# Performance work log

Hardware: AMD Instinct MI355X
Metric: run time of the kernel (lower is better)

Reference implementation:

```python
import jax, jax.numpy as jnp
import numpy as np

T = 2048          # num tokens (prefill)
H = 4096          # hidden_size
NH = 32           # num query heads
NKV = 8           # num kv heads (GQA)
HD = H // NH      # head_dim = 128
BASE = 1000000.0  # rope_theta
NEG = -1e30


def _rope(x, positions):
    # NeoX-style rotary embedding (vLLM default). x: [T, nh, HD]
    half = HD // 2
    inv_freq = 1.0 / (BASE ** (jnp.arange(half, dtype=jnp.float32) / half))
    freqs = positions.astype(jnp.float32)[:, None] * inv_freq  # [T, half]
    cos = jnp.concatenate([jnp.cos(freqs), jnp.cos(freqs)], -1)[:, None, :]
    sin = jnp.concatenate([jnp.sin(freqs), jnp.sin(freqs)], -1)[:, None, :]
    rot = jnp.concatenate([-x[..., half:], x[..., :half]], -1)
    return x * cos + rot * sin


def setup_inputs() -> dict:
    key = jax.random.key(0)
    k1, k2, k3 = jax.random.split(key, 3)
    hidden_states = jax.random.normal(k1, (T, H), jnp.float32)
    wqkv = jax.random.normal(k2, (H, (NH + 2 * NKV) * HD), jnp.float32) * 0.02
    wo = jax.random.normal(k3, (NH * HD, H), jnp.float32) * 0.02
    positions = jnp.arange(T, dtype=jnp.int32)
    return {"positions": positions, "hidden_states": hidden_states,
            "wqkv": wqkv, "wo": wo}


def reference(positions, hidden_states, wqkv, wo):
    # fused QKV projection
    qkv = hidden_states @ wqkv                      # [T, (NH+2*NKV)*HD]
    q, k, v = jnp.split(qkv, [NH * HD, NH * HD + NKV * HD], axis=-1)
    q = q.reshape(T, NH, HD)
    k = k.reshape(T, NKV, HD)
    v = v.reshape(T, NKV, HD)
    # inline RoPE on q, k
    q = _rope(q, positions)
    k = _rope(k, positions)
    # GQA: expand kv heads to query heads
    rep = NH // NKV
    k = jnp.repeat(k, rep, axis=1)                  # [T, NH, HD]
    v = jnp.repeat(v, rep, axis=1)
    # causal scaled dot-product attention (prefill path of PagedAttention)
    scores = jnp.einsum('qhd,khd->hqk', q, k) * (HD ** -0.5)  # [NH, T, T]
    causal = positions[:, None] >= positions[None, :]          # [T, T]
    scores = jnp.where(causal[None, :, :], scores, NEG)
    probs = jax.nn.softmax(scores, axis=-1)
    attn = jnp.einsum('hqk,khd->qhd', probs, v).reshape(T, NH * HD)
    return attn @ wo
```

## Files before the change

kernel.cpp:

```cpp
#include <hip/hip_runtime.h>
#include <hip/hip_bf16.h>

typedef __attribute__((ext_vector_type(8))) short bf16x8;
typedef __attribute__((ext_vector_type(4))) float f32x4;
typedef unsigned short u16;

#define T_TOK 2048
#define HID 4096
#define NH 32
#define NKV 8
#define HD 128
#define QKVN 6144
#define KOFF 4096
#define VOFF 5120
#define QSCALE (0.08838834764831845f * 1.4426950408889634f)
#define THR_LOG2 11.0f

static __device__ __forceinline__ float bf2f(u16 x) {
    union { float f; unsigned u; } v; v.u = ((unsigned)x) << 16; return v.f;
}
static __device__ __forceinline__ u16 f2bf(float f) {
    union { float f; unsigned u; } v; v.f = f;
    unsigned u = v.u;
    unsigned r = (u + 0x7fff + ((u >> 16) & 1)) >> 16;
    return (u16)r;
}

static __device__ __forceinline__ void gload16(const u16* g, u16* l) {
    __builtin_amdgcn_global_load_lds((const __attribute__((address_space(1))) void*)g,
                                     (__attribute__((address_space(3))) void*)l, 16, 0, 0);
}

#define VMC(n) asm volatile("s_waitcnt vmcnt(%0)" :: "i"(n) : "memory")
#define LGKM0() asm volatile("s_waitcnt lgkmcnt(0)" ::: "memory")
#define BAR() __builtin_amdgcn_s_barrier()
#define SCHB() __builtin_amdgcn_sched_barrier(0)

__global__ __launch_bounds__(256) void prepk(const float* __restrict__ hs, u16* __restrict__ hsb,
                                             const float* __restrict__ wqkv, u16* __restrict__ wqkvT,
                                             const float* __restrict__ wo, u16* __restrict__ woT) {
    __shared__ float tile[64][65];
    int by = blockIdx.y;
    int tid = threadIdx.x;
    if (by >= 64) {
        int b = blockIdx.x + 160 * (by - 64);
        for (int i = b * 256 + tid; i < (T_TOK * HID / 4); i += 1280 * 256) {
            float4 v = ((const float4*)hs)[i];
            ushort4 o;
            o.x = f2bf(v.x); o.y = f2bf(v.y); o.z = f2bf(v.z); o.w = f2bf(v.w);
            ((ushort4*)hsb)[i] = o;
        }
        return;
    }
    int bx = blockIdx.x;
    const float* in; u16* out; int C, c0;
    if (bx < 96) { in = wqkv; out = wqkvT; C = QKVN; c0 = bx * 64; }
    else         { in = wo;   out = woT;   C = HID;  c0 = (bx - 96) * 64; }
    int R = HID;
    int r0 = by * 64;
#pragma unroll
    for (int it = 0; it < 4; ++it) {
        int ci = it * 256 + tid;
        int r = ci >> 4, c4 = (ci & 15) * 4;
        float4 v = *(const float4*)&in[(size_t)(r0 + r) * C + c0 + c4];
        tile[r][c4 + 0] = v.x; tile[r][c4 + 1] = v.y; tile[r][c4 + 2] = v.z; tile[r][c4 + 3] = v.w;
    }
    __syncthreads();
#pragma unroll
    for (int it = 0; it < 4; ++it) {
        int ci = it * 256 + tid;
        int c = ci >> 4, rq = (ci & 15) * 4;
        ushort4 o;
        o.x = f2bf(tile[rq + 0][c]); o.y = f2bf(tile[rq + 1][c]);
        o.z = f2bf(tile[rq + 2][c]); o.w = f2bf(tile[rq + 3][c]);
        *(ushort4*)&out[(size_t)(c0 + c) * R + r0 + rq] = o;
    }
}

template <int BN, int OUTF32>
__global__ __launch_bounds__(512) void gemm8p(const u16* __restrict__ A, const u16* __restrict__ Bt,
                                              void* __restrict__ Cout, int M, int N, int K) {
    constexpr int BM = 256, BK = 32;
    constexpr int WN = BN / 2;
    constexpr int NF = WN / 16;
    constexpr int BCH = BN / 16;
    constexpr int CA = 2 + (BCH + 7) / 8;
    constexpr int CB = 2 + BCH / 8;
    constexpr int ABUF = BM * BK;
    constexpr int BBUF = BN * BK;
    constexpr int BUFSZ = ABUF + BBUF;

    __shared__ __attribute__((aligned(16))) u16 lds[4 * BUFSZ];

    int bid = blockIdx.x;
    int m0 = ((bid >> 3) & 7) * BM;
    int n0 = ((bid & 7) * 4 + (bid >> 6)) * BN;
    int tid = threadIdx.x, lane = tid & 63, wid = tid >> 6;
    int wm = wid >> 1, wn = wid & 1;
    int l15 = lane & 15, g4 = lane >> 4;
    int srow = lane >> 2;
    int sslot = (lane & 3) ^ ((lane >> 3) & 3);
    int swz = (g4 ^ ((l15 >> 1) & 3)) * 8;
    int NK = K / BK;
    bool shortw = (CA != CB) && (wid >= 4);

    auto STAGE = [&](int kt, int c) {
        u16* base = &lds[(kt & 3) * BUFSZ];
        size_t kcol = (size_t)kt * BK + sslot * 8;
        if (c < 2) {
            int ch = wid * 2 + c;
            gload16(&A[(size_t)(m0 + ch * 16 + srow) * K + kcol], base + ch * 512);
        } else {
            int ch = (c - 2) * 8 + wid;
            if (ch < BCH)
                gload16(&Bt[(size_t)(n0 + ch * 16 + srow) * K + kcol], base + ABUF + ch * 512);
        }
    };

    f32x4 acc[4][NF];
#pragma unroll
    for (int i = 0; i < 4; ++i)
#pragma unroll
        for (int j = 0; j < NF; ++j) acc[i][j] = (f32x4){0.f, 0.f, 0.f, 0.f};

    for (int t = 0; t < 3; ++t)
        for (int c = 0; c < CA; ++c) STAGE(t, c);
    if (shortw) VMC(2 * CB); else VMC(2 * CA);
    BAR(); SCHB();

    for (int g = 0; g < NK; ++g) {
        const u16* ab = &lds[(g & 3) * BUFSZ];
        const u16* bb = ab + ABUF;

        bf16x8 bfr[NF], af0, af1;
#pragma unroll
        for (int j = 0; j < NF; ++j)
            bfr[j] = *(const bf16x8*)&bb[(wn * WN + j * 16 + l15) * BK + swz];
        af0 = *(const bf16x8*)&ab[(wm * 64 + 0 * 16 + l15) * BK + swz];
        af1 = *(const bf16x8*)&ab[(wm * 64 + 1 * 16 + l15) * BK + swz];
        if (g + 3 < NK) {
            STAGE(g + 3, 0); STAGE(g + 3, 1);
        }
        __builtin_amdgcn_s_setprio(1);
#pragma unroll
        for (int j = 0; j < NF; ++j) {
            acc[0][j] = __builtin_amdgcn_mfma_f32_16x16x32_bf16(af0, bfr[j], acc[0][j], 0, 0, 0);
            acc[1][j] = __builtin_amdgcn_mfma_f32_16x16x32_bf16(af1, bfr[j], acc[1][j], 0, 0, 0);
        }
        __builtin_amdgcn_s_setprio(0);

        bf16x8 af2, af3;
        af2 = *(const bf16x8*)&ab[(wm * 64 + 2 * 16 + l15) * BK + swz];
        af3 = *(const bf16x8*)&ab[(wm * 64 + 3 * 16 + l15) * BK + swz];
        if (g + 3 < NK) {
#pragma unroll
            for (int c = 2; c < CA; ++c) STAGE(g + 3, c);
        }
        __builtin_amdgcn_s_setprio(1);
#pragma unroll
        for (int j = 0; j < NF; ++j) {
            acc[2][j] = __builtin_amdgcn_mfma_f32_16x16x32_bf16(af2, bfr[j], acc[2][j], 0, 0, 0);
            acc[3][j] = __builtin_amdgcn_mfma_f32_16x16x32_bf16(af3, bfr[j], acc[3][j], 0, 0, 0);
        }
        __builtin_amdgcn_s_setprio(0);

        if (g < NK - 3)       { if (shortw) VMC(2 * CB); else VMC(2 * CA); }
        else if (g == NK - 3) { if (shortw) VMC(CB);     else VMC(CA); }
        else if (g == NK - 2) VMC(0);
        BAR(); SCHB();
    }

#pragma unroll
    for (int mi = 0; mi < 4; ++mi)
#pragma unroll
        for (int j = 0; j < NF; ++j)
#pragma unroll
            for (int i = 0; i < 4; ++i) {
                int row = m0 + wm * 64 + mi * 16 + g4 * 4 + i;
                int col = n0 + wn * WN + j * 16 + l15;
                float v = acc[mi][j][i];
                if (OUTF32) ((float*)Cout)[(size_t)row * N + col] = v;
                else        ((u16*)Cout)[(size_t)row * N + col] = f2bf(v);
            }
}

template <int BN, int OUTF32>
__global__ __launch_bounds__(512) void gemm4p(const u16* __restrict__ A, const u16* __restrict__ Bt,
                                              void* __restrict__ Cout, int M, int N, int K) {
    constexpr int NF = BN / 64;
    constexpr int LB = BN / 128;
    constexpr int DBUF = (128 + BN) * 64;
    constexpr int BHALF = (BN / 2) * 64;
    __shared__ __attribute__((aligned(16))) u16 lds[2 * DBUF];

    int bid = blockIdx.x;
    int m0 = ((bid >> 3) & 15) * 128;
    int n0 = ((bid & 7) * 2 + (bid >> 7)) * BN;
    int tid = threadIdx.x, lane = tid & 63, wid = tid >> 6;
    int wm = wid >> 2, wn = wid & 3;
    int l15 = lane & 15, g4 = lane >> 4;
    int sw = l15 & 7;
    int srow = tid >> 3;
    int sslot8 = (((tid & 7) ^ ((tid >> 3) & 7))) * 8;
    int brow0 = (wn & 1) * (BN / 4);
    int NK = K / 64;

    auto STAGE_A = [&](int kt, int h) {
        gload16(&A[(size_t)(m0 + h * 64 + srow) * K + kt * 64 + sslot8],
                &lds[(kt & 1) * DBUF + h * 4096 + wid * 512]);
    };
    auto STAGE_B = [&](int kt, int bh) {
#pragma unroll
        for (int it = 0; it < LB; ++it)
            gload16(&Bt[(size_t)(n0 + bh * (BN / 2) + it * 64 + srow) * K + kt * 64 + sslot8],
                    &lds[(kt & 1) * DBUF + 8192 + bh * BHALF + it * 4096 + wid * 512]);
    };

    f32x4 acc[4][NF];
#pragma unroll
    for (int i = 0; i < 4; ++i)
#pragma unroll
        for (int j = 0; j < NF; ++j) acc[i][j] = (f32x4){0.f, 0.f, 0.f, 0.f};

    STAGE_A(0, 0); STAGE_A(0, 1); STAGE_B(0, 0); STAGE_B(0, 1);
    STAGE_A(1, 0); STAGE_A(1, 1); STAGE_B(1, 0); STAGE_B(1, 1);
    VMC(2 + 2 * LB);
    BAR(); SCHB();

    for (int g = 0; g < NK; ++g) {
        const u16* dd = &lds[(g & 1) * DBUF];
        const u16* aw = dd + wm * 4096;
        const u16* bw = dd + 8192 + (wn >> 1) * BHALF;
        bool mid = (g > 0) && (g + 1 < NK);
        bf16x8 bfr[NF], af0, af1;

#pragma unroll
        for (int nf = 0; nf < NF; ++nf)
            bfr[nf] = *(const bf16x8*)&bw[(brow0 + nf * 16 + l15) * 64 + ((g4 ^ sw) * 8)];
        af0 = *(const bf16x8*)&aw[(0 * 16 + l15) * 64 + ((g4 ^ sw) * 8)];
        af1 = *(const bf16x8*)&aw[(1 * 16 + l15) * 64 + ((g4 ^ sw) * 8)];
        if (mid) STAGE_A(g + 1, 0);
        BAR(); LGKM0();
        __builtin_amdgcn_s_setprio(1);
#pragma unroll
        for (int nf = 0; nf < NF; ++nf) {
            acc[0][nf] = __builtin_amdgcn_mfma_f32_16x16x32_bf16(af0, bfr[nf], acc[0][nf], 0, 0, 0);
            acc[1][nf] = __builtin_amdgcn_mfma_f32_16x16x32_bf16(af1, bfr[nf], acc[1][nf], 0, 0, 0);
        }
        __builtin_amdgcn_s_setprio(0);
        BAR();

        af0 = *(const bf16x8*)&aw[(2 * 16 + l15) * 64 + ((g4 ^ sw) * 8)];
        af1 = *(const bf16x8*)&aw[(3 * 16 + l15) * 64 + ((g4 ^ sw) * 8)];
        if (mid) STAGE_B(g + 1, 1);
        BAR(); LGKM0();
        __builtin_amdgcn_s_setprio(1);
#pragma unroll
        for (int nf = 0; nf < NF; ++nf) {
            acc[2][nf] = __builtin_amdgcn_mfma_f32_16x16x32_bf16(af0, bfr[nf], acc[2][nf], 0, 0, 0);
            acc[3][nf] = __builtin_amdgcn_mfma_f32_16x16x32_bf16(af1, bfr[nf], acc[3][nf], 0, 0, 0);
        }
        __builtin_amdgcn_s_setprio(0);
        BAR();

#pragma unroll
        for (int nf = 0; nf < NF; ++nf)
            bfr[nf] = *(const bf16x8*)&bw[(brow0 + nf * 16 + l15) * 64 + (((4 + g4) ^ sw) * 8)];
        af0 = *(const bf16x8*)&aw[(0 * 16 + l15) * 64 + (((4 + g4) ^ sw) * 8)];
        af1 = *(const bf16x8*)&aw[(1 * 16 + l15) * 64 + (((4 + g4) ^ sw) * 8)];
        if (mid) STAGE_A(g + 1, 1);
        BAR(); LGKM0();
        __builtin_amdgcn_s_setprio(1);
#pragma unroll
        for (int nf = 0; nf < NF; ++nf) {
            acc[0][nf] = __builtin_amdgcn_mfma_f32_16x16x32_bf16(af0, bfr[nf], acc[0][nf], 0, 0, 0);
            acc[1][nf] = __builtin_amdgcn_mfma_f32_16x16x32_bf16(af1, bfr[nf], acc[1][nf], 0, 0, 0);
        }
        __builtin_amdgcn_s_setprio(0);
        BAR();

        af0 = *(const bf16x8*)&aw[(2 * 16 + l15) * 64 + (((4 + g4) ^ sw) * 8)];
        af1 = *(const bf16x8*)&aw[(3 * 16 + l15) * 64 + (((4 + g4) ^ sw) * 8)];
        if (g + 2 < NK) STAGE_B(g + 2, 0);
        BAR(); LGKM0();
        __builtin_amdgcn_s_setprio(1);
#pragma unroll
        for (int nf = 0; nf < NF; ++nf) {
            acc[2][nf] = __builtin_amdgcn_mfma_f32_16x16x32_bf16(af0, bfr[nf], acc[2][nf], 0, 0, 0);
            acc[3][nf] = __builtin_amdgcn_mfma_f32_16x16x32_bf16(af1, bfr[nf], acc[3][nf], 0, 0, 0);
        }
        __builtin_amdgcn_s_setprio(0);
        if (g <= NK - 3)      VMC(LB);
        else if (g == NK - 2) VMC(0);
        BAR(); SCHB();
    }

#pragma unroll
    for (int mf = 0; mf < 4; ++mf)
#pragma unroll
        for (int nf = 0; nf < NF; ++nf)
#pragma unroll
            for (int i = 0; i < 4; ++i) {
                int row = m0 + wm * 64 + mf * 16 + g4 * 4 + i;
                int col = n0 + wn * (BN / 4) + nf * 16 + l15;
                float v = acc[mf][nf][i];
                if (OUTF32) ((float*)Cout)[(size_t)row * N + col] = v;
                else        ((u16*)Cout)[(size_t)row * N + col] = f2bf(v);
            }
}

__global__ __launch_bounds__(256) void ropevtk(u16* __restrict__ qkvb, const int* __restrict__ positions,
                                               u16* __restrict__ vT) {
    __shared__ __attribute__((aligned(16))) u16 tile[64][136];
    int bx = blockIdx.x;
    int tid = threadIdx.x;
    if (bx < 2048) {
        __shared__ float cs_[64], sn_[64];
        int t = bx;
        float pos = (float)positions[t];
        if (tid < 64) {
            int d = tid;
            float inv = exp2f(-(float)d * (19.931568569324174f / 64.0f));
            float fr = pos * inv;
            cs_[d] = cosf(fr);
            sn_[d] = sinf(fr);
        }
        __syncthreads();
#pragma unroll
        for (int it = 0; it < 10; ++it) {
            int ci = it * 256 + tid;
            int hh = ci >> 6, d = ci & 63;
            int base = (hh < NH) ? hh * HD : KOFF + (hh - NH) * HD;
            size_t off = (size_t)t * QKVN + base + d;
            float x1 = bf2f(qkvb[off]);
            float x2 = bf2f(qkvb[off + 64]);
            float s = sn_[d], c = cs_[d];
            float y1 = x1 * c - x2 * s;
            float y2 = x2 * c + x1 * s;
            if (hh < NH) { y1 *= QSCALE; y2 *= QSCALE; }
            qkvb[off]      = f2bf(y1);
            qkvb[off + 64] = f2bf(y2);
        }
        return;
    }
    int idx = bx - 2048;
    int kvh = idx >> 5, t0 = (idx & 31) * 64;
#pragma unroll
    for (int it = 0; it < 4; ++it) {
        int ci = it * 256 + tid;
        int r = ci >> 4, c8 = (ci & 15) * 8;
        *(bf16x8*)&tile[r][c8] = *(const bf16x8*)&qkvb[(size_t)(t0 + r) * QKVN + VOFF + kvh * HD + c8];
    }
    __syncthreads();
#pragma unroll
    for (int it = 0; it < 4; ++it) {
        int ci = it * 256 + tid;
        int d = ci >> 3, tc = (ci & 7) * 8;
        union { bf16x8 v; u16 u[8]; } o;
#pragma unroll
        for (int e = 0; e < 8; ++e) o.u[e] = tile[tc + e][d];
        *(bf16x8*)&vT[((size_t)kvh * HD + d) * T_TOK + t0 + tc] = o.v;
    }
}

__global__ __launch_bounds__(512) void attnk(const u16* __restrict__ qkvb, const u16* __restrict__ vT,
                                             u16* __restrict__ attnb) {
    __shared__ __attribute__((aligned(16))) u16 kt_[64 * 132];
    __shared__ __attribute__((aligned(16))) u16 vt_[128 * 68];
    __shared__ __attribute__((aligned(16))) u16 pl_[8 * 16 * 68];
    int h = blockIdx.x, qt = 15 - blockIdx.y;
    int kvh = h >> 2;
    int q0 = qt * 128;
    int tid = threadIdx.x, lane = tid & 63, wid = tid >> 6;
    int l15 = lane & 15, g = lane >> 4;

    const u16* kbase = qkvb + KOFF + (size_t)kvh * HD;
    const u16* vbase = vT + (size_t)kvh * HD * T_TOK;

    bf16x8 qf[4];
    int qrow = q0 + wid * 16 + l15;
#pragma unroll
    for (int ks = 0; ks < 4; ++ks)
        qf[ks] = *(const bf16x8*)&qkvb[(size_t)qrow * QKVN + h * HD + ks * 32 + g * 8];

    f32x4 o[8];
#pragma unroll
    for (int df = 0; df < 8; ++df) o[df] = (f32x4){0.f, 0.f, 0.f, 0.f};
    float m_run[4], l_run[4];
#pragma unroll
    for (int i = 0; i < 4; ++i) { m_run[i] = -3.0e38f; l_run[i] = 0.f; }

    int NT = 2 * qt + 2;

    bf16x8 kreg[2], vreg[2];
#pragma unroll
    for (int it = 0; it < 2; ++it) {
        int gi = it * 512 + tid;
        kreg[it] = *(const bf16x8*)&kbase[(size_t)(gi >> 4) * QKVN + (gi & 15) * 8];
        vreg[it] = *(const bf16x8*)&vbase[(size_t)(gi >> 3) * T_TOK + (gi & 7) * 8];
    }
#pragma unroll
    for (int it = 0; it < 2; ++it) {
        int gi = it * 512 + tid;
        *(bf16x8*)&kt_[(gi >> 4) * 132 + (gi & 15) * 8] = kreg[it];
        *(bf16x8*)&vt_[(gi >> 3) * 68 + (gi & 7) * 8] = vreg[it];
    }
#pragma unroll
    for (int it = 0; it < 2; ++it) {
        int gi = it * 512 + tid;
        kreg[it] = *(const bf16x8*)&kbase[(size_t)(64 + (gi >> 4)) * QKVN + (gi & 15) * 8];
        vreg[it] = *(const bf16x8*)&vbase[(size_t)(gi >> 3) * T_TOK + 64 + (gi & 7) * 8];
    }
    __syncthreads();

    for (int kt2 = 0; kt2 < NT; ++kt2) {
        int kvb = kt2 * 64;
        bool active = (kvb <= q0 + wid * 16 + 15);
        bool diag   = (kvb + 63 > q0 + wid * 16);

        if (active) {
            f32x4 s[4];
#pragma unroll
            for (int nf = 0; nf < 4; ++nf) s[nf] = (f32x4){0.f, 0.f, 0.f, 0.f};
            __builtin_amdgcn_s_setprio(1);
#pragma unroll
            for (int ks = 0; ks < 4; ++ks) {
#pragma unroll
                for (int nf = 0; nf < 4; ++nf) {
                    bf16x8 bfr = *(const bf16x8*)&kt_[(nf * 16 + l15) * 132 + ks * 32 + g * 8];
                    s[nf] = __builtin_amdgcn_mfma_f32_16x16x32_bf16(qf[ks], bfr, s[nf], 0, 0, 0);
                }
            }
            __builtin_amdgcn_s_setprio(0);

            float mloc[4];
#pragma unroll
            for (int i = 0; i < 4; ++i) {
                int qr = q0 + wid * 16 + g * 4 + i;
                float mx = -3.0e38f;
#pragma unroll
                for (int nf = 0; nf < 4; ++nf) {
                    float v = s[nf][i];
                    if (diag) {
                        int kvc = kvb + nf * 16 + l15;
                        v = (kvc <= qr) ? v : -1.0e30f;
                        s[nf][i] = v;
                    }
                    mx = fmaxf(mx, v);
                }
                mloc[i] = mx;
            }

            int ok = 1;
#pragma unroll
            for (int i = 0; i < 4; ++i) ok &= (mloc[i] <= m_run[i] + THR_LOG2) ? 1 : 0;
            if (!__all(ok)) {
                float mrow[4];
#pragma unroll
                for (int i = 0; i < 4; ++i) mrow[i] = mloc[i];
#pragma unroll
                for (int dd = 1; dd < 16; dd <<= 1)
#pragma unroll
                    for (int i = 0; i < 4; ++i) mrow[i] = fmaxf(mrow[i], __shfl_xor(mrow[i], dd));
                float alpha[4];
#pragma unroll
                for (int i = 0; i < 4; ++i) {
                    float mnew = fmaxf(m_run[i], mrow[i]);
                    alpha[i] = exp2f(m_run[i] - mnew);
                    m_run[i] = mnew;
                    l_run[i] *= alpha[i];
                }
#pragma unroll
                for (int df = 0; df < 8; ++df)
#pragma unroll
                    for (int i = 0; i < 4; ++i) o[df][i] *= alpha[i];
            }

#pragma unroll
            for (int nf = 0; nf < 4; ++nf)
#pragma unroll
                for (int i = 0; i < 4; ++i) {
                    float p = exp2f(s[nf][i] - m_run[i]);
                    l_run[i] += p;
                    pl_[wid * 1088 + (g * 4 + i) * 68 + nf * 16 + l15] = f2bf(p);
                }

            __builtin_amdgcn_s_setprio(1);
#pragma unroll
            for (int ks2 = 0; ks2 < 2; ++ks2) {
                bf16x8 af = *(const bf16x8*)&pl_[wid * 1088 + l15 * 68 + ks2 * 32 + g * 8];
#pragma unroll
                for (int df = 0; df < 8; ++df) {
                    bf16x8 bfr = *(const bf16x8*)&vt_[(df * 16 + l15) * 68 + ks2 * 32 + g * 8];
                    o[df] = __builtin_amdgcn_mfma_f32_16x16x32_bf16(af, bfr, o[df], 0, 0, 0);
                }
            }
            __builtin_amdgcn_s_setprio(0);
        }

        if (kt2 < NT - 1) {
            __syncthreads();
#pragma unroll
            for (int it = 0; it < 2; ++it) {
                int gi = it * 512 + tid;
                *(bf16x8*)&kt_[(gi >> 4) * 132 + (gi & 15) * 8] = kreg[it];
                *(bf16x8*)&vt_[(gi >> 3) * 68 + (gi & 7) * 8] = vreg[it];
            }
            int ktl = (kt2 + 2 < NT) ? kt2 + 2 : NT - 1;
#pragma unroll
            for (int it = 0; it < 2; ++it) {
                int gi = it * 512 + tid;
                kreg[it] = *(const bf16x8*)&kbase[(size_t)(ktl * 64 + (gi >> 4)) * QKVN + (gi & 15) * 8];
                vreg[it] = *(const bf16x8*)&vbase[(size_t)(gi >> 3) * T_TOK + ktl * 64 + (gi & 7) * 8];
            }
            __syncthreads();
        }
    }

#pragma unroll
    for (int dd = 1; dd < 16; dd <<= 1)
#pragma unroll
        for (int i = 0; i < 4; ++i) l_run[i] += __shfl_xor(l_run[i], dd);

#pragma unroll
    for (int df = 0; df < 8; ++df)
#pragma unroll
        for (int i = 0; i < 4; ++i) {
            int qr = q0 + wid * 16 + g * 4 + i;
            int col = h * HD + df * 16 + l15;
            attnb[(size_t)qr * (NH * HD) + col] = f2bf(o[df][i] / l_run[i]);
        }
}

extern "C" void kernel_launch(void* const* d_in, const int* in_sizes, int n_in,
                              void* d_out, int out_size, void* d_ws, size_t ws_size,
                              hipStream_t stream) {
    const int*   positions = (const int*)d_in[0];
    const float* hs        = (const float*)d_in[1];
    const float* wqkv      = (const float*)d_in[2];
    const float* wo        = (const float*)d_in[3];
    float* out = (float*)d_out;

    char* ws = (char*)d_ws;
    u16* hsb   = (u16*)(ws);
    u16* wqkvT = (u16*)(ws + 16777216);
    u16* woT   = (u16*)(ws + 16777216 + 50331648);
    u16* qkvb  = (u16*)(ws + 16777216 + 50331648 + 33554432);
    u16* vT    = (u16*)(ws + 16777216 + 50331648 + 33554432 + 25165824);
    u16* attnb = hsb;

    prepk<<<dim3(160, 72), 256, 0, stream>>>(hs, hsb, wqkv, wqkvT, wo, woT);

    gemm8p<192, 0><<<dim3(256), 512, 0, stream>>>(hsb, wqkvT, qkvb, T_TOK, QKVN, HID);

    ropevtk<<<dim3(2048 + 256), 256, 0, stream>>>(qkvb, positions, vT);

    attnk<<<dim3(NH, 16), 512, 0, stream>>>(qkvb, vT, attnb);

    gemm4p<256, 1><<<dim3(256), 512, 0, stream>>>(attnb, woT, out, T_TOK, HID, HID);
}
```

Before: 313.0 us.

## Split attention KV range across two blocks and merge with a combine kernel

The causal attention kernel now splits each query tile's key range into two halves handled by separate blocks (grid z=2). Each block writes a partial normalized output plus its running max and sum, and a new combine kernel merges the halves with log-sum-exp weights. This doubles the block count and shortens the longest per-block loop, which improves load balance and occupancy across CUs. The cost is an extra launch and an extra round trip of partial outputs through memory, and the partials are stored in bf16 before combining.

```diff
diff --git a/kernel.cpp b/kernel.cpp
--- a/kernel.cpp
+++ b/kernel.cpp
@@ -364,16 +364,20 @@
 }
 
 __global__ __launch_bounds__(512) void attnk(const u16* __restrict__ qkvb, const u16* __restrict__ vT,
-                                             u16* __restrict__ attnb) {
+                                             u16* __restrict__ Opart, float* __restrict__ mlp) {
     __shared__ __attribute__((aligned(16))) u16 kt_[64 * 132];
     __shared__ __attribute__((aligned(16))) u16 vt_[128 * 68];
     __shared__ __attribute__((aligned(16))) u16 pl_[8 * 16 * 68];
     int h = blockIdx.x, qt = 15 - blockIdx.y;
+    int z = blockIdx.z;
     int kvh = h >> 2;
     int q0 = qt * 128;
     int tid = threadIdx.x, lane = tid & 63, wid = tid >> 6;
     int l15 = lane & 15, g = lane >> 4;
 
+    int tb = z * (qt + 1);
+    int te = tb + qt + 1;
+
     const u16* kbase = qkvb + KOFF + (size_t)kvh * HD;
     const u16* vbase = vT + (size_t)kvh * HD * T_TOK;
 
@@ -390,14 +394,12 @@
 #pragma unroll
     for (int i = 0; i < 4; ++i) { m_run[i] = -3.0e38f; l_run[i] = 0.f; }
 
-    int NT = 2 * qt + 2;
-
     bf16x8 kreg[2], vreg[2];
 #pragma unroll
     for (int it = 0; it < 2; ++it) {
         int gi = it * 512 + tid;
-        kreg[it] = *(const bf16x8*)&kbase[(size_t)(gi >> 4) * QKVN + (gi & 15) * 8];
-        vreg[it] = *(const bf16x8*)&vbase[(size_t)(gi >> 3) * T_TOK + (gi & 7) * 8];
+        kreg[it] = *(const bf16x8*)&kbase[(size_t)(tb * 64 + (gi >> 4)) * QKVN + (gi & 15) * 8];
+        vreg[it] = *(const bf16x8*)&vbase[(size_t)(gi >> 3) * T_TOK + tb * 64 + (gi & 7) * 8];
     }
 #pragma unroll
     for (int it = 0; it < 2; ++it) {
@@ -405,15 +407,18 @@
         *(bf16x8*)&kt_[(gi >> 4) * 132 + (gi & 15) * 8] = kreg[it];
         *(bf16x8*)&vt_[(gi >> 3) * 68 + (gi & 7) * 8] = vreg[it];
     }
-#pragma unroll
-    for (int it = 0; it < 2; ++it) {
-        int gi = it * 512 + tid;
-        kreg[it] = *(const bf16x8*)&kbase[(size_t)(64 + (gi >> 4)) * QKVN + (gi & 15) * 8];
-        vreg[it] = *(const bf16x8*)&vbase[(size_t)(gi >> 3) * T_TOK + 64 + (gi & 7) * 8];
+    {
+        int ktl = (tb + 1 < te) ? tb + 1 : te - 1;
+#pragma unroll
+        for (int it = 0; it < 2; ++it) {
+            int gi = it * 512 + tid;
+            kreg[it] = *(const bf16x8*)&kbase[(size_t)(ktl * 64 + (gi >> 4)) * QKVN + (gi & 15) * 8];
+            vreg[it] = *(const bf16x8*)&vbase[(size_t)(gi >> 3) * T_TOK + ktl * 64 + (gi & 7) * 8];
+        }
     }
     __syncthreads();
 
-    for (int kt2 = 0; kt2 < NT; ++kt2) {
+    for (int kt2 = tb; kt2 < te; ++kt2) {
         int kvb = kt2 * 64;
         bool active = (kvb <= q0 + wid * 16 + 15);
         bool diag   = (kvb + 63 > q0 + wid * 16);
@@ -498,7 +503,7 @@
             __builtin_amdgcn_s_setprio(0);
         }
 
-        if (kt2 < NT - 1) {
+        if (kt2 < te - 1) {
             __syncthreads();
 #pragma unroll
             for (int it = 0; it < 2; ++it) {
@@ -506,7 +511,7 @@
                 *(bf16x8*)&kt_[(gi >> 4) * 132 + (gi & 15) * 8] = kreg[it];
                 *(bf16x8*)&vt_[(gi >> 3) * 68 + (gi & 7) * 8] = vreg[it];
             }
-            int ktl = (kt2 + 2 < NT) ? kt2 + 2 : NT - 1;
+            int ktl = (kt2 + 2 < te) ? kt2 + 2 : te - 1;
 #pragma unroll
             for (int it = 0; it < 2; ++it) {
                 int gi = it * 512 + tid;
@@ -522,14 +527,55 @@
 #pragma unroll
         for (int i = 0; i < 4; ++i) l_run[i] += __shfl_xor(l_run[i], dd);
 
+    float linv[4];
+#pragma unroll
+    for (int i = 0; i < 4; ++i) linv[i] = (l_run[i] > 0.f) ? 1.f / l_run[i] : 0.f;
+
 #pragma unroll
     for (int df = 0; df < 8; ++df)
 #pragma unroll
         for (int i = 0; i < 4; ++i) {
             int qr = q0 + wid * 16 + g * 4 + i;
             int col = h * HD + df * 16 + l15;
-            attnb[(size_t)qr * (NH * HD) + col] = f2bf(o[df][i] / l_run[i]);
-        }
+            Opart[(size_t)(z * T_TOK + qr) * (NH * HD) + col] = f2bf(o[df][i] * linv[i]);
+        }
+    if (l15 == 0) {
+#pragma unroll
+        for (int i = 0; i < 4; ++i) {
+            int qr = q0 + wid * 16 + g * 4 + i;
+            size_t mi = ((size_t)(z * T_TOK + qr) * NH + h) * 2;
+            mlp[mi] = m_run[i];
+            mlp[mi + 1] = l_run[i];
+        }
+    }
+}
+
+__global__ __launch_bounds__(256) void combk(const u16* __restrict__ Opart, const float* __restrict__ mlp,
+                                             u16* __restrict__ attnb) {
+    int qr = blockIdx.x;
+    int tid = threadIdx.x;
+    int h = tid >> 3, e0 = (tid & 7) * 16;
+    size_t m1i = ((size_t)qr * NH + h) * 2;
+    size_t m2i = ((size_t)(T_TOK + qr) * NH + h) * 2;
+    float m1 = mlp[m1i], l1 = mlp[m1i + 1];
+    float m2 = mlp[m2i], l2 = mlp[m2i + 1];
+    float mm = fmaxf(m1, m2);
+    float w1 = exp2f(m1 - mm) * l1;
+    float w2 = exp2f(m2 - mm) * l2;
+    float inv = 1.f / (w1 + w2);
+    const u16* p1 = &Opart[(size_t)qr * (NH * HD) + h * HD + e0];
+    const u16* p2 = &Opart[(size_t)(T_TOK + qr) * (NH * HD) + h * HD + e0];
+    u16* po = &attnb[(size_t)qr * (NH * HD) + h * HD + e0];
+#pragma unroll
+    for (int c = 0; c < 2; ++c) {
+        union { bf16x8 v; u16 u[8]; } a, b, r;
+        a.v = *(const bf16x8*)&p1[c * 8];
+        b.v = *(const bf16x8*)&p2[c * 8];
+#pragma unroll
+        for (int j = 0; j < 8; ++j)
+            r.u[j] = f2bf((w1 * bf2f(a.u[j]) + w2 * bf2f(b.u[j])) * inv);
+        *(bf16x8*)&po[c * 8] = r.v;
+    }
 }
 
 extern "C" void kernel_launch(void* const* d_in, const int* in_sizes, int n_in,
@@ -548,6 +594,8 @@
     u16* qkvb  = (u16*)(ws + 16777216 + 50331648 + 33554432);
     u16* vT    = (u16*)(ws + 16777216 + 50331648 + 33554432 + 25165824);
     u16* attnb = hsb;
+    u16*   Opart = wqkvT;
+    float* mlp   = (float*)(ws + 16777216 + 33554432);
 
     prepk<<<dim3(160, 72), 256, 0, stream>>>(hs, hsb, wqkv, wqkvT, wo, woT);
 
@@ -555,7 +603,8 @@
 
     ropevtk<<<dim3(2048 + 256), 256, 0, stream>>>(qkvb, positions, vT);
 
-    attnk<<<dim3(NH, 16), 512, 0, stream>>>(qkvb, vT, attnb);
+    attnk<<<dim3(NH, 16, 2), 512, 0, stream>>>(qkvb, vT, Opart, mlp);
+    combk<<<dim3(T_TOK), 256, 0, stream>>>(Opart, mlp, attnb);
 
     gemm4p<256, 1><<<dim3(256), 512, 0, stream>>>(attnb, woT, out, T_TOK, HID, HID);
 }
```

Result: slower. 327.9 us (+4.8%).
